# Kernel tuning notes

Measured on AMD Instinct MI355X. Metric: run time of the kernel, lower is better.

## Reference

```python
import jax, jax.numpy as jnp
import numpy as np

B, N, D = 16, 2048, 512   # batch, tokens, latent dim
K = 8192                  # codebook size


def setup_inputs() -> dict:
    key = jax.random.key(0)
    k1, k2 = jax.random.split(key)
    ze = jax.random.normal(k1, (B, N, D), dtype=jnp.float32)
    codebook = jax.random.normal(k2, (K, D), dtype=jnp.float32)
    return {"ze": ze, "codebook": codebook}


def reference(ze, codebook):
    # Pairwise squared distances: ||ze||^2 + ||c||^2 - 2 ze.c  -> [B, N, K]
    sq_norm = (
        jnp.sum(ze ** 2, axis=-1, keepdims=True)
        + jnp.sum(codebook ** 2, axis=1)
        - 2.0 * jnp.einsum("bnd,kd->bnk", ze, codebook)
    )
    argmin = jnp.argmin(sq_norm, axis=-1)  # [B, N]
    zq = codebook[argmin]                  # gather -> [B, N, D]
    return zq
```

## Files before the change

### kernel.cpp

```cpp
#include <hip/hip_runtime.h>
#include <cfloat>

#define TOKENS 32768
#define DDIM   512
#define KCODES 8192

#define CAP    160
#define MARGIN 2.0f

#define ZEBF_OFF   0
#define CBBF_OFF   (TOKENS * DDIM * 2)
#define CNORM_OFF  (CBBF_OFF + KCODES * DDIM * 2)
#define CNT_OFF    (CNORM_OFF + KCODES * 4)
#define CANDI_OFF  (CNT_OFF + TOKENS * 4)
#define CANDS_OFF  (CANDI_OFF + TOKENS * CAP * 4)
#define WS_REQ     ((size_t)(CANDS_OFF + TOKENS * CAP * 4))

typedef short bf16x8 __attribute__((ext_vector_type(8)));
typedef float f32x4  __attribute__((ext_vector_type(4)));

__device__ __forceinline__ void gld16(const void* g, void* l) {
    __builtin_amdgcn_global_load_lds(
        (const __attribute__((address_space(1))) void*)g,
        (__attribute__((address_space(3))) void*)l,
        16, 0, 0);
}

__device__ __forceinline__ unsigned short f2bf(float f) {
    union { float f; unsigned int u; } v; v.f = f;
    unsigned int u = v.u;
    return (unsigned short)((u + 0x7fffu + ((u >> 16) & 1u)) >> 16);
}

__global__ __launch_bounds__(256) void convert_kernel(const float* __restrict__ src,
                                                      unsigned short* __restrict__ dst,
                                                      int n8) {
    int i = blockIdx.x * 256 + threadIdx.x;
    if (i >= n8) return;
    float4 a = ((const float4*)src)[i * 2];
    float4 b = ((const float4*)src)[i * 2 + 1];
    bf16x8 o;
    o[0] = (short)f2bf(a.x); o[1] = (short)f2bf(a.y);
    o[2] = (short)f2bf(a.z); o[3] = (short)f2bf(a.w);
    o[4] = (short)f2bf(b.x); o[5] = (short)f2bf(b.y);
    o[6] = (short)f2bf(b.z); o[7] = (short)f2bf(b.w);
    *(bf16x8*)&dst[(size_t)i * 8] = o;
}

__global__ __launch_bounds__(256) void cnorm_kernel(const float* __restrict__ cb,
                                                    float* __restrict__ cnorm) {
    int row  = blockIdx.x * 4 + (threadIdx.x >> 6);
    int lane = threadIdx.x & 63;
    const float* r = cb + (size_t)row * DDIM;
    float s = 0.f;
    #pragma unroll
    for (int d = lane; d < DDIM; d += 64) { float v = r[d]; s += v * v; }
    #pragma unroll
    for (int off = 32; off > 0; off >>= 1) s += __shfl_down(s, off, 64);
    if (lane == 0) cnorm[row] = s;
}

__global__ __launch_bounds__(256, 3) void vq_mfma_kernel(
        const unsigned short* __restrict__ zebf,
        const unsigned short* __restrict__ cbbf,
        const float* __restrict__ cnorm,
        int* __restrict__ cnt,
        int* __restrict__ candI,
        float* __restrict__ candS) {
    __shared__ unsigned short Ab[128 * 64];
    __shared__ unsigned short Bb[128 * 64];
    __shared__ float smin[2][128];

    const int tid  = threadIdx.x;
    const int w    = tid >> 6;
    const int lane = tid & 63;
    const int wr   = w >> 1;
    const int wc   = w & 1;

    const int bid      = blockIdx.x;
    const int xcd      = bid & 7;
    const int loc      = bid >> 3;
    const int panel    = loc >> 8;
    const int l2i      = loc & 255;
    const int tb_local = l2i >> 3;
    const int cb_local = l2i & 7;
    const int token_blk = tb_local * 8 + xcd;
    const int code_blk  = panel * 8 + cb_local;

    const int tok0  = token_blk * 128;
    const int code0 = code_blk * 128;

    int ldsOff[4], offA[4], offB[4];
    #pragma unroll
    for (int i = 0; i < 4; ++i) {
        int L    = ((i * 4 + w) * 1024) + lane * 16;
        int row  = L >> 7;
        int phys = (L >> 4) & 7;
        int slog = phys ^ (row & 7);
        ldsOff[i] = L;
        offA[i] = (tok0 + row) * DDIM + slog * 8;
        offB[i] = (code0 + row) * DDIM + slog * 8;
    }

    const int s0 = lane >> 4;
    int aOff[4], bOff[4];
    #pragma unroll
    for (int rt = 0; rt < 4; ++rt) {
        int row  = wr * 64 + rt * 16 + (lane & 15);
        aOff[rt] = row * 128 + ((s0 ^ (row & 7)) * 16);
    }
    #pragma unroll
    for (int ct = 0; ct < 4; ++ct) {
        int row  = wc * 64 + ct * 16 + (lane & 15);
        bOff[ct] = row * 128 + ((s0 ^ (row & 7)) * 16);
    }

    f32x4 acc[4][4];
    const f32x4 zero = {0.f, 0.f, 0.f, 0.f};
    #pragma unroll
    for (int i = 0; i < 4; ++i)
        #pragma unroll
        for (int j = 0; j < 4; ++j) acc[i][j] = zero;

    for (int dk = 0; dk < DDIM; dk += 64) {
        __syncthreads();
        #pragma unroll
        for (int i = 0; i < 4; ++i) {
            gld16(zebf + (size_t)(offA[i] + dk), (char*)Ab + ldsOff[i]);
            gld16(cbbf + (size_t)(offB[i] + dk), (char*)Bb + ldsOff[i]);
        }
        __syncthreads();

        #pragma unroll
        for (int kk = 0; kk < 2; ++kk) {
            bf16x8 af[4], bfr[4];
            #pragma unroll
            for (int rt = 0; rt < 4; ++rt)
                af[rt] = *(const bf16x8*)((const char*)Ab + (aOff[rt] ^ (kk * 64)));
            #pragma unroll
            for (int ct = 0; ct < 4; ++ct)
                bfr[ct] = *(const bf16x8*)((const char*)Bb + (bOff[ct] ^ (kk * 64)));
            #pragma unroll
            for (int rt = 0; rt < 4; ++rt)
                #pragma unroll
                for (int ct = 0; ct < 4; ++ct)
                    acc[rt][ct] = __builtin_amdgcn_mfma_f32_16x16x32_bf16(
                        af[rt], bfr[ct], acc[rt][ct], 0, 0, 0);
        }
    }

    float cn[4];
    #pragma unroll
    for (int ct = 0; ct < 4; ++ct)
        cn[ct] = cnorm[code0 + wc * 64 + ct * 16 + (lane & 15)];

    float rm[4][4];
    #pragma unroll
    for (int rt = 0; rt < 4; ++rt)
        #pragma unroll
        for (int r = 0; r < 4; ++r) {
            float m = cn[0] - 2.f * acc[rt][0][r];
            #pragma unroll
            for (int ct = 1; ct < 4; ++ct)
                m = fminf(m, cn[ct] - 2.f * acc[rt][ct][r]);
            #pragma unroll
            for (int off = 1; off < 16; off <<= 1)
                m = fminf(m, __shfl_xor(m, off, 64));
            rm[rt][r] = m;
            if ((lane & 15) == 0)
                smin[wc][wr * 64 + rt * 16 + (lane >> 4) * 4 + r] = m;
        }
    __syncthreads();

    #pragma unroll
    for (int rt = 0; rt < 4; ++rt)
        #pragma unroll
        for (int r = 0; r < 4; ++r) {
            int tl = wr * 64 + rt * 16 + (lane >> 4) * 4 + r;
            float mo  = smin[1 - wc][tl];
            float thr = fminf(rm[rt][r], mo) + MARGIN;
            int token = tok0 + tl;
            #pragma unroll
            for (int ct = 0; ct < 4; ++ct) {
                float s = cn[ct] - 2.f * acc[rt][ct][r];
                if (s <= thr) {
                    int pos = atomicAdd(&cnt[token], 1);
                    if (pos < CAP) {
                        candI[(size_t)token * CAP + pos] = code0 + wc * 64 + ct * 16 + (lane & 15);
                        candS[(size_t)token * CAP + pos] = s;
                    }
                }
            }
        }
}

__global__ __launch_bounds__(64) void rescore_kernel(
        const float* __restrict__ ze, const float* __restrict__ cb,
        const float* __restrict__ cnorm, const int* __restrict__ cnt,
        const int* __restrict__ candI, const float* __restrict__ candS,
        float* __restrict__ out) {
    const int t    = blockIdx.x;
    const int lane = threadIdx.x;

    float4 za = *(const float4*)&ze[(size_t)t * DDIM + lane * 8];
    float4 zb = *(const float4*)&ze[(size_t)t * DDIM + lane * 8 + 4];

    int n = cnt[t];
    bool ovf = (n > CAP) || (n <= 0);

    float best = FLT_MAX;
    int   bidx = 0x7fffffff;

    if (!ovf) {
        float m = FLT_MAX;
        for (int e = lane; e < n; e += 64)
            m = fminf(m, candS[(size_t)t * CAP + e]);
        #pragma unroll
        for (int off = 32; off > 0; off >>= 1)
            m = fminf(m, __shfl_xor(m, off, 64));
        float thr = m + MARGIN;

        for (int base = 0; base < n; base += 64) {
            int e = base + lane;
            int myI = 0; float sv = FLT_MAX;
            if (e < n) { myI = candI[(size_t)t * CAP + e]; sv = candS[(size_t)t * CAP + e]; }
            unsigned long long mask = __ballot(e < n && sv <= thr);
            while (mask) {
                int b = __ffsll((long long)mask) - 1;
                mask &= mask - 1;
                int code = __shfl(myI, b, 64);
                const float* row = cb + (size_t)code * DDIM + lane * 8;
                float4 ca = *(const float4*)row;
                float4 cc = *(const float4*)(row + 4);
                float d = za.x*ca.x + za.y*ca.y + za.z*ca.z + za.w*ca.w
                        + zb.x*cc.x + zb.y*cc.y + zb.z*cc.z + zb.w*cc.w;
                #pragma unroll
                for (int off = 32; off > 0; off >>= 1) d += __shfl_xor(d, off, 64);
                float s = cnorm[code] - 2.f * d;
                if (s < best || (s == best && code < bidx)) { best = s; bidx = code; }
            }
        }
    } else {
        for (int code = 0; code < KCODES; ++code) {
            const float* row = cb + (size_t)code * DDIM + lane * 8;
            float4 ca = *(const float4*)row;
            float4 cc = *(const float4*)(row + 4);
            float d = za.x*ca.x + za.y*ca.y + za.z*ca.z + za.w*ca.w
                    + zb.x*cc.x + zb.y*cc.y + zb.z*cc.z + zb.w*cc.w;
            #pragma unroll
            for (int off = 32; off > 0; off >>= 1) d += __shfl_xor(d, off, 64);
            float s = cnorm[code] - 2.f * d;
            if (s < best || (s == best && code < bidx)) { best = s; bidx = code; }
        }
    }

    const float* src = cb + (size_t)bidx * DDIM + lane * 8;
    float4 o0 = *(const float4*)src;
    float4 o1 = *(const float4*)(src + 4);
    *(float4*)&out[(size_t)t * DDIM + lane * 8]     = o0;
    *(float4*)&out[(size_t)t * DDIM + lane * 8 + 4] = o1;
}

#define TM 64
#define TN 64
#define BK 32
#define LDS_STRIDE (TM + 4)

__global__ __launch_bounds__(256) void vq_fallback_kernel(const float* __restrict__ ze,
                                                          const float* __restrict__ cb,
                                                          const float* __restrict__ cnorm,
                                                          float* __restrict__ out) {
    __shared__ float At[BK][LDS_STRIDE];
    __shared__ float Bt[BK][LDS_STRIDE];
    __shared__ float rv[TM][16];
    __shared__ int   ri[TM][16];
    __shared__ int   best_s[TM];

    const int tid = threadIdx.x;
    const int tx  = tid & 15;
    const int ty  = tid >> 4;
    const int token_base = blockIdx.x * TM;
    const int sc = tid & 31;
    const int sr = tid >> 5;

    float bestv[4] = {FLT_MAX, FLT_MAX, FLT_MAX, FLT_MAX};
    int   besti[4] = {0, 0, 0, 0};

    for (int ctile = 0; ctile < KCODES; ctile += TN) {
        float acc[4][4] = {{0.f}};
        for (int dk = 0; dk < DDIM; dk += BK) {
            __syncthreads();
            #pragma unroll
            for (int p = 0; p < 8; ++p) {
                int r = p * 8 + sr;
                At[sc][r] = ze[(size_t)(token_base + r) * DDIM + dk + sc];
                Bt[sc][r] = cb[(size_t)(ctile + r) * DDIM + dk + sc];
            }
            __syncthreads();
            #pragma unroll
            for (int d = 0; d < BK; ++d) {
                float a[4], b[4];
                *(float4*)a = *(const float4*)&At[d][ty * 4];
                *(float4*)b = *(const float4*)&Bt[d][tx * 4];
                #pragma unroll
                for (int i = 0; i < 4; ++i)
                    #pragma unroll
                    for (int j = 0; j < 4; ++j)
                        acc[i][j] += a[i] * b[j];
            }
        }
        #pragma unroll
        for (int j = 0; j < 4; ++j) {
            int code = ctile + tx * 4 + j;
            float cnv = cnorm[code];
            #pragma unroll
            for (int i = 0; i < 4; ++i) {
                float s = cnv - 2.f * acc[i][j];
                if (s < bestv[i]) { bestv[i] = s; besti[i] = code; }
            }
        }
    }
    #pragma unroll
    for (int i = 0; i < 4; ++i) {
        rv[ty * 4 + i][tx] = bestv[i];
        ri[ty * 4 + i][tx] = besti[i];
    }
    __syncthreads();
    if (tid < TM) {
        float bv = rv[tid][0]; int bi = ri[tid][0];
        #pragma unroll
        for (int x = 1; x < 16; ++x) {
            float v = rv[tid][x]; int ix = ri[tid][x];
            if (v < bv || (v == bv && ix < bi)) { bv = v; bi = ix; }
        }
        best_s[tid] = bi;
    }
    __syncthreads();
    const int gr   = tid >> 7;
    const int gcol = (tid & 127) * 4;
    for (int rr = 0; rr < TM; rr += 2) {
        int tk  = rr + gr;
        int src = best_s[tk];
        float4 v = *(const float4*)&cb[(size_t)src * DDIM + gcol];
        *(float4*)&out[(size_t)(token_base + tk) * DDIM + gcol] = v;
    }
}

extern "C" void kernel_launch(void* const* d_in, const int* in_sizes, int n_in,
                              void* d_out, int out_size, void* d_ws, size_t ws_size,
                              hipStream_t stream) {
    const float* ze = (const float*)d_in[0];
    const float* cb = (const float*)d_in[1];
    float* out      = (float*)d_out;

    if (ws_size < WS_REQ) {
        float* cnorm = (float*)d_ws;
        cnorm_kernel<<<KCODES / 4, 256, 0, stream>>>(cb, cnorm);
        vq_fallback_kernel<<<TOKENS / TM, 256, 0, stream>>>(ze, cb, cnorm, out);
        return;
    }

    char* ws = (char*)d_ws;
    unsigned short* zebf = (unsigned short*)(ws + ZEBF_OFF);
    unsigned short* cbbf = (unsigned short*)(ws + CBBF_OFF);
    float* cnorm = (float*)(ws + CNORM_OFF);
    int*   cnt   = (int*)(ws + CNT_OFF);
    int*   candI = (int*)(ws + CANDI_OFF);
    float* candS = (float*)(ws + CANDS_OFF);

    convert_kernel<<<(TOKENS * DDIM / 8) / 256, 256, 0, stream>>>(ze, zebf, TOKENS * DDIM / 8);
    convert_kernel<<<(KCODES * DDIM / 8) / 256, 256, 0, stream>>>(cb, cbbf, KCODES * DDIM / 8);
    cnorm_kernel<<<KCODES / 4, 256, 0, stream>>>(cb, cnorm);
    hipMemsetAsync(cnt, 0, TOKENS * sizeof(int), stream);

    vq_mfma_kernel<<<(TOKENS / 128) * (KCODES / 128), 256, 0, stream>>>(
        zebf, cbbf, cnorm, cnt, candI, candS);

    rescore_kernel<<<TOKENS, 64, 0, stream>>>(ze, cb, cnorm, cnt, candI, candS, out);
}
```

Measured before the change: 732.0 us.

## Triple-buffer the MFMA K-loop and split rescore across four waves

The GEMM main loop changes from a single-buffered 64-wide K tile with two barriers per step to a three-stage ring of 32-wide K tiles. Global-to-LDS loads are issued two chunks ahead and gated by explicit vmcnt waits, so memory latency overlaps the MFMA work, and the LDS swizzle is reworked for the narrower rows. The rescore kernel now runs four waves per token, each scanning a share of the candidates (or of the full codebook on overflow), then reduces through shared memory. This adds wave-level parallelism to rescoring but brings a block barrier and depends on hand-tuned vmcnt counts matching the number of issued loads.

```diff
diff --git a/kernel.cpp b/kernel.cpp
--- a/kernel.cpp
+++ b/kernel.cpp
@@ -24,6 +24,12 @@
         (const __attribute__((address_space(1))) void*)g,
         (__attribute__((address_space(3))) void*)l,
         16, 0, 0);
+}
+
+__device__ __forceinline__ void fence_barrier() {
+    __builtin_amdgcn_sched_barrier(0);
+    __builtin_amdgcn_s_barrier();
+    __builtin_amdgcn_sched_barrier(0);
 }
 
 __device__ __forceinline__ unsigned short f2bf(float f) {
@@ -67,8 +73,8 @@
         int* __restrict__ cnt,
         int* __restrict__ candI,
         float* __restrict__ candS) {
-    __shared__ unsigned short Ab[128 * 64];
-    __shared__ unsigned short Bb[128 * 64];
+    __shared__ unsigned short Ab[3][128 * 32];
+    __shared__ unsigned short Bb[3][128 * 32];
     __shared__ float smin[2][128];
 
     const int tid  = threadIdx.x;
@@ -90,16 +96,16 @@
     const int tok0  = token_blk * 128;
     const int code0 = code_blk * 128;
 
-    int ldsOff[4], offA[4], offB[4];
-    #pragma unroll
-    for (int i = 0; i < 4; ++i) {
-        int L    = ((i * 4 + w) * 1024) + lane * 16;
-        int row  = L >> 7;
-        int phys = (L >> 4) & 7;
-        int slog = phys ^ (row & 7);
-        ldsOff[i] = L;
-        offA[i] = (tok0 + row) * DDIM + slog * 8;
-        offB[i] = (code0 + row) * DDIM + slog * 8;
+    int ldsOff[2], offA[2], offB[2];
+    #pragma unroll
+    for (int p = 0; p < 2; ++p) {
+        int L    = p * 4096 + tid * 16;
+        int row  = L >> 6;
+        int phys = (L >> 4) & 3;
+        int slog = phys ^ ((row >> 1) & 3);
+        ldsOff[p] = L;
+        offA[p] = (tok0  + row) * DDIM + slog * 8;
+        offB[p] = (code0 + row) * DDIM + slog * 8;
     }
 
     const int s0 = lane >> 4;
@@ -107,12 +113,12 @@
     #pragma unroll
     for (int rt = 0; rt < 4; ++rt) {
         int row  = wr * 64 + rt * 16 + (lane & 15);
-        aOff[rt] = row * 128 + ((s0 ^ (row & 7)) * 16);
+        aOff[rt] = row * 32 + (s0 ^ ((row >> 1) & 3)) * 8;
     }
     #pragma unroll
     for (int ct = 0; ct < 4; ++ct) {
         int row  = wc * 64 + ct * 16 + (lane & 15);
-        bOff[ct] = row * 128 + ((s0 ^ (row & 7)) * 16);
+        bOff[ct] = row * 32 + (s0 ^ ((row >> 1) & 3)) * 8;
     }
 
     f32x4 acc[4][4];
@@ -122,32 +128,54 @@
         #pragma unroll
         for (int j = 0; j < 4; ++j) acc[i][j] = zero;
 
-    for (int dk = 0; dk < DDIM; dk += 64) {
-        __syncthreads();
-        #pragma unroll
-        for (int i = 0; i < 4; ++i) {
-            gld16(zebf + (size_t)(offA[i] + dk), (char*)Ab + ldsOff[i]);
-            gld16(cbbf + (size_t)(offB[i] + dk), (char*)Bb + ldsOff[i]);
-        }
-        __syncthreads();
-
-        #pragma unroll
-        for (int kk = 0; kk < 2; ++kk) {
-            bf16x8 af[4], bfr[4];
-            #pragma unroll
-            for (int rt = 0; rt < 4; ++rt)
-                af[rt] = *(const bf16x8*)((const char*)Ab + (aOff[rt] ^ (kk * 64)));
+    auto STAGE = [&](int buf, int ck) {
+        int dk = ck * 32;
+        #pragma unroll
+        for (int p = 0; p < 2; ++p) {
+            gld16(zebf + (size_t)(offA[p] + dk), (char*)Ab[buf] + ldsOff[p]);
+            gld16(cbbf + (size_t)(offB[p] + dk), (char*)Bb[buf] + ldsOff[p]);
+        }
+    };
+
+    auto COMPUTE = [&](int buf) {
+        const unsigned short* A = Ab[buf];
+        const unsigned short* B = Bb[buf];
+        bf16x8 af[4], bfr[4];
+        #pragma unroll
+        for (int rt = 0; rt < 4; ++rt) af[rt]  = *(const bf16x8*)(A + aOff[rt]);
+        #pragma unroll
+        for (int ct = 0; ct < 4; ++ct) bfr[ct] = *(const bf16x8*)(B + bOff[ct]);
+        #pragma unroll
+        for (int rt = 0; rt < 4; ++rt)
             #pragma unroll
             for (int ct = 0; ct < 4; ++ct)
-                bfr[ct] = *(const bf16x8*)((const char*)Bb + (bOff[ct] ^ (kk * 64)));
-            #pragma unroll
-            for (int rt = 0; rt < 4; ++rt)
-                #pragma unroll
-                for (int ct = 0; ct < 4; ++ct)
-                    acc[rt][ct] = __builtin_amdgcn_mfma_f32_16x16x32_bf16(
-                        af[rt], bfr[ct], acc[rt][ct], 0, 0, 0);
-        }
-    }
+                acc[rt][ct] = __builtin_amdgcn_mfma_f32_16x16x32_bf16(
+                    af[rt], bfr[ct], acc[rt][ct], 0, 0, 0);
+    };
+
+    const int NCHUNK = DDIM / 32;
+
+    STAGE(0, 0);
+    STAGE(1, 1);
+    #pragma unroll 1
+    for (int t = 0; t < NCHUNK - 2; ++t) {
+        STAGE((t + 2) % 3, t + 2);
+        __builtin_amdgcn_sched_barrier(0);
+        asm volatile("s_waitcnt vmcnt(8)" ::: "memory");
+        __builtin_amdgcn_sched_barrier(0);
+        fence_barrier();
+        COMPUTE(t % 3);
+        fence_barrier();
+    }
+    asm volatile("s_waitcnt vmcnt(4)" ::: "memory");
+    __builtin_amdgcn_sched_barrier(0);
+    fence_barrier();
+    COMPUTE((NCHUNK - 2) % 3);
+    fence_barrier();
+    asm volatile("s_waitcnt vmcnt(0)" ::: "memory");
+    __builtin_amdgcn_sched_barrier(0);
+    fence_barrier();
+    COMPUTE((NCHUNK - 1) % 3);
 
     float cn[4];
     #pragma unroll
@@ -194,13 +222,18 @@
         }
 }
 
-__global__ __launch_bounds__(64) void rescore_kernel(
+__global__ __launch_bounds__(256) void rescore_kernel(
         const float* __restrict__ ze, const float* __restrict__ cb,
         const float* __restrict__ cnorm, const int* __restrict__ cnt,
         const int* __restrict__ candI, const float* __restrict__ candS,
         float* __restrict__ out) {
     const int t    = blockIdx.x;
-    const int lane = threadIdx.x;
+    const int tid  = threadIdx.x;
+    const int v    = tid >> 6;
+    const int lane = tid & 63;
+
+    __shared__ float sbest[4];
+    __shared__ int   sidx[4];
 
     float4 za = *(const float4*)&ze[(size_t)t * DDIM + lane * 8];
     float4 zb = *(const float4*)&ze[(size_t)t * DDIM + lane * 8 + 4];
@@ -220,7 +253,7 @@
             m = fminf(m, __shfl_xor(m, off, 64));
         float thr = m + MARGIN;
 
-        for (int base = 0; base < n; base += 64) {
+        for (int base = v * 64; base < n; base += 256) {
             int e = base + lane;
             int myI = 0; float sv = FLT_MAX;
             if (e < n) { myI = candI[(size_t)t * CAP + e]; sv = candS[(size_t)t * CAP + e]; }
@@ -241,7 +274,7 @@
             }
         }
     } else {
-        for (int code = 0; code < KCODES; ++code) {
+        for (int code = v; code < KCODES; code += 4) {
             const float* row = cb + (size_t)code * DDIM + lane * 8;
             float4 ca = *(const float4*)row;
             float4 cc = *(const float4*)(row + 4);
@@ -254,11 +287,20 @@
         }
     }
 
-    const float* src = cb + (size_t)bidx * DDIM + lane * 8;
-    float4 o0 = *(const float4*)src;
-    float4 o1 = *(const float4*)(src + 4);
-    *(float4*)&out[(size_t)t * DDIM + lane * 8]     = o0;
-    *(float4*)&out[(size_t)t * DDIM + lane * 8 + 4] = o1;
+    if (lane == 0) { sbest[v] = best; sidx[v] = bidx; }
+    __syncthreads();
+
+    float fb = sbest[0]; int fi = sidx[0];
+    #pragma unroll
+    for (int k = 1; k < 4; ++k) {
+        float s = sbest[k]; int ix = sidx[k];
+        if (s < fb || (s == fb && ix < fi)) { fb = s; fi = ix; }
+    }
+
+    if (tid < 128) {
+        float4 o = *(const float4*)&cb[(size_t)fi * DDIM + tid * 4];
+        *(float4*)&out[(size_t)t * DDIM + tid * 4] = o;
+    }
 }
 
 #define TM 64
@@ -376,5 +418,5 @@
     vq_mfma_kernel<<<(TOKENS / 128) * (KCODES / 128), 256, 0, stream>>>(
         zebf, cbbf, cnorm, cnt, candI, candS);
 
-    rescore_kernel<<<TOKENS, 64, 0, stream>>>(ze, cb, cnorm, cnt, candI, candS, out);
-}
+    rescore_kernel<<<TOKENS, 256, 0, stream>>>(ze, cb, cnorm, cnt, candI, candS, out);
+}
```

After: 803.6 us. 9.8% more time.
